# Kernel optimization log

Hardware: AMD Instinct MI355X
Metric: run time of the kernel (lower is better)

The kernel has to match this reference:

```python
import jax, jax.numpy as jnp
import numpy as np

NUM_HEADS = 16


def rotate_half(x):
    half = x.shape[-1] // 2
    return jnp.concatenate([-x[..., half:], x[..., :half]], axis=-1)


def setup_inputs() -> dict:
    key = jax.random.key(0)
    k0, k1, k2 = jax.random.split(key, 3)
    S, DIM, H = 16384, 1280, NUM_HEADS
    D = DIM // H            # 80
    G, L = 16, 1024         # 16 images, 1024 patch tokens each (S = G*L)

    hidden_states = jax.random.normal(k0, (S, DIM), dtype=jnp.float32) * 0.02

    # RoPE tables over packed positions
    pos = jnp.arange(S, dtype=jnp.float32)
    inv_freq = 1.0 / (10000.0 ** (jnp.arange(0, D, 2, dtype=jnp.float32) / D))
    freqs = pos[:, None] * inv_freq[None, :]          # [S, D/2]
    emb = jnp.concatenate([freqs, freqs], axis=-1)    # [S, D]
    cos = jnp.cos(emb)
    sin = jnp.sin(emb)

    cu_seqlens = (jnp.arange(G + 1, dtype=jnp.int32) * L)

    w_qkv = jax.random.normal(k1, (DIM, 3 * DIM), dtype=jnp.float32) * 0.02
    b_qkv = jnp.zeros((3 * DIM,), dtype=jnp.float32)
    w_proj = jax.random.normal(k2, (DIM, DIM), dtype=jnp.float32) * 0.02
    b_proj = jnp.zeros((DIM,), dtype=jnp.float32)

    return {
        "hidden_states": hidden_states,
        "cos": cos,
        "sin": sin,
        "w_qkv": w_qkv,
        "b_qkv": b_qkv,
        "w_proj": w_proj,
        "b_proj": b_proj,
        "cu_seqlens": cu_seqlens,
    }


def reference(hidden_states, cos, sin, w_qkv, b_qkv, w_proj, b_proj, cu_seqlens):
    S, DIM = hidden_states.shape
    H = NUM_HEADS
    D = DIM // H
    G = cu_seqlens.shape[0] - 1   # equal-length segments
    L = S // G

    qkv = (hidden_states @ w_qkv + b_qkv).reshape(S, 3, H, D)
    q, k, v = qkv[:, 0], qkv[:, 1], qkv[:, 2]   # [S, H, D]

    # RoPE (computed in fp32 as in source)
    c = cos[:, None, :]
    s = sin[:, None, :]
    q = q * c + rotate_half(q) * s
    k = k * c + rotate_half(k) * s

    # Source applies head_dim**-0.5 on q AND SDPA's default head_dim**-0.5,
    # so effective scale is head_dim**-1.
    scale = 1.0 / D

    qg = q.reshape(G, L, H, D)
    kg = k.reshape(G, L, H, D)
    vg = v.reshape(G, L, H, D)

    scores = jnp.einsum('glhd,gmhd->ghlm', qg, kg) * scale  # [G,H,L,L]
    attn = jax.nn.softmax(scores, axis=-1)
    out = jnp.einsum('ghlm,gmhd->glhd', attn, vg)           # [G,L,H,D]
    out = out.reshape(S, H * D)
    return out @ w_proj + b_proj
```

## Files before the change

### kernel.cpp

```cpp
#include <hip/hip_runtime.h>
#include <cmath>

#define SEQ   16384
#define DIMV  1280
#define NH    16
#define HD    80
#define NG    16
#define GL    1024
#define LDQKV (3*DIMV)

typedef short s16x8 __attribute__((ext_vector_type(8)));
typedef float f32x4 __attribute__((ext_vector_type(4)));

__device__ __forceinline__ unsigned short f2bf(float f) {
    union { float f; unsigned int u; } v; v.f = f;
    unsigned int u = v.u;
    return (unsigned short)((u + 0x7FFFu + ((u >> 16) & 1u)) >> 16);
}
__device__ __forceinline__ float bf2f(unsigned short h) {
    union { unsigned int u; float f; } v; v.u = ((unsigned int)h) << 16;
    return v.f;
}
__device__ __forceinline__ unsigned int pack2(float a, float b) {
    return (unsigned int)f2bf(a) | ((unsigned int)f2bf(b) << 16);
}
__device__ __forceinline__ void gload_lds16(const void* g, void* l) {
    __builtin_amdgcn_global_load_lds(
        (const __attribute__((address_space(1))) unsigned int*)g,
        (__attribute__((address_space(3))) unsigned int*)l,
        16, 0, 0);
}

__global__ __launch_bounds__(256) void convert_bf16_kernel(
    const float* __restrict__ src, unsigned short* __restrict__ dst, int n)
{
    int i = (blockIdx.x * 256 + threadIdx.x) * 8;
    if (i >= n) return;
    float4 a = *(const float4*)&src[i];
    float4 b = *(const float4*)&src[i + 4];
    uint4 o;
    o.x = pack2(a.x, a.y); o.y = pack2(a.z, a.w);
    o.z = pack2(b.x, b.y); o.w = pack2(b.z, b.w);
    *(uint4*)&dst[i] = o;
}

__global__ __launch_bounds__(256) void transpose_bf16_kernel(
    const float* __restrict__ W, unsigned short* __restrict__ WT,
    int Kdim, int N)
{
    __shared__ float tile[32][33];
    const int bx = blockIdx.x * 32;
    const int by = blockIdx.y * 32;
    const int tx = threadIdx.x & 31, ty = threadIdx.x >> 5;
#pragma unroll
    for (int j = 0; j < 4; ++j)
        tile[ty + j * 8][tx] = W[(size_t)(by + ty + j * 8) * N + bx + tx];
    __syncthreads();
#pragma unroll
    for (int j = 0; j < 4; ++j)
        WT[(size_t)(bx + ty + j * 8) * Kdim + by + tx] =
            f2bf(tile[tx][ty + j * 8]);
}

__global__ __launch_bounds__(256) void vtranspose_kernel(
    const unsigned short* __restrict__ qkv, unsigned short* __restrict__ vT)
{
    __shared__ unsigned short tile[128][88];
    const int t  = threadIdx.x;
    const int l0 = blockIdx.x * 128;
    const int gh = blockIdx.y;
    const int g  = gh >> 4, h = gh & 15;

#pragma unroll
    for (int s = 0; s < 5; ++s) {
        int i = t + s * 256;
        int row = i / 10, c = i % 10;
        *(uint4*)&tile[row][c * 8] = *(const uint4*)
            &qkv[(size_t)(g * GL + l0 + row) * LDQKV + 2 * DIMV + h * HD + c * 8];
    }
    __syncthreads();

#pragma unroll
    for (int s = 0; s < 5; ++s) {
        int i = t + s * 256;
        int d = i / 16, c16 = i % 16;
        uint4 o;
        o.x = (unsigned int)tile[c16 * 8 + 0][d] | ((unsigned int)tile[c16 * 8 + 1][d] << 16);
        o.y = (unsigned int)tile[c16 * 8 + 2][d] | ((unsigned int)tile[c16 * 8 + 3][d] << 16);
        o.z = (unsigned int)tile[c16 * 8 + 4][d] | ((unsigned int)tile[c16 * 8 + 5][d] << 16);
        o.w = (unsigned int)tile[c16 * 8 + 6][d] | ((unsigned int)tile[c16 * 8 + 7][d] << 16);
        *(uint4*)&vT[((size_t)gh * HD + d) * GL + l0 + c16 * 8] = o;
    }
}

template <bool BF16_OUT>
__global__ __launch_bounds__(512, 2) void gemm256_kernel(
    const unsigned short* __restrict__ A,
    const unsigned short* __restrict__ BT,
    const float* __restrict__ bias,
    void* __restrict__ C, int ldc, int K)
{
    __shared__ unsigned short As0[256 * 64], Bs0[256 * 64];
    __shared__ unsigned short As1[256 * 64], Bs1[256 * 64];

    const int t    = threadIdx.x;
    const int w    = t >> 6, lane = t & 63;
    const int wm   = w >> 2, wn = w & 3;
    const int gr   = lane >> 4, c15 = lane & 15;

    const int dd  = blockIdx.y * gridDim.x + blockIdx.x;
    const int cpx = (gridDim.x * gridDim.y) >> 3;
    const int sw  = (dd & 7) * cpx + (dd >> 3);
    const int bn  = (sw / gridDim.y) * 256;
    const int bm  = (sw % gridDim.y) * 256;

    const unsigned short* Ab = A  + (size_t)bm * K;
    const unsigned short* Bb = BT + (size_t)bn * K;
    const int NT = K >> 6;

    size_t soff[2]; int dstoff[2];
#pragma unroll
    for (int i = 0; i < 2; ++i) {
        int idx = t + i * 512, r = idx >> 3, blk = idx & 7;
        int cb  = blk ^ (r & 7);
        soff[i]   = ((size_t)r * K + cb * 8) * 2;
        dstoff[i] = idx * 16;
    }
    auto stage = [&](const unsigned short* src, unsigned short* ldsb,
                     int kt, int hh) {
#pragma unroll
        for (int i = 0; i < 2; ++i)
            gload_lds16((const char*)src + soff[i]
                            + (size_t)hh * ((size_t)128 * K * 2)
                            + (size_t)kt * 128,
                        (char*)ldsb + hh * 16384 + dstoff[i]);
    };

    f32x4 acc[8][4];
#pragma unroll
    for (int m = 0; m < 8; ++m)
#pragma unroll
        for (int n = 0; n < 4; ++n) acc[m][n] = (f32x4){0.f, 0.f, 0.f, 0.f};

    stage(Ab, As0, 0, 0); stage(Ab, As0, 0, 1);
    stage(Bb, Bs0, 0, 0); stage(Bb, Bs0, 0, 1);
    if (NT > 1) {
        stage(Bb, Bs1, 1, 0); stage(Bb, Bs1, 1, 1);
        asm volatile("s_waitcnt vmcnt(4)" ::: "memory");
    } else {
        asm volatile("s_waitcnt vmcnt(0)" ::: "memory");
    }
    __builtin_amdgcn_s_barrier();

    int cur = 0;
    for (int kt = 0; kt < NT; ++kt) {
        const unsigned short* Ac = cur ? As1 : As0;
        const unsigned short* Bc = cur ? Bs1 : Bs0;
        unsigned short* An  = cur ? As0 : As1;
        unsigned short* Bcw = cur ? Bs1 : Bs0;

        s16x8 bf[4][2];
#pragma unroll
        for (int p = 0; p < 4; ++p) {
            if (p == 0) {
#pragma unroll
                for (int n = 0; n < 4; ++n)
#pragma unroll
                    for (int k = 0; k < 2; ++k) {
                        int row = wn * 64 + n * 16 + c15;
                        bf[n][k] = *(const s16x8*)((const char*)Bc + row * 128
                                       + ((k * 64 + gr * 16) ^ ((row & 7) << 4)));
                    }
            }
            s16x8 af[2][2];
#pragma unroll
            for (int mi = 0; mi < 2; ++mi)
#pragma unroll
                for (int k = 0; k < 2; ++k) {
                    int row = wm * 128 + p * 32 + mi * 16 + c15;
                    af[mi][k] = *(const s16x8*)((const char*)Ac + row * 128
                                    + ((k * 64 + gr * 16) ^ ((row & 7) << 4)));
                }
            if (p == 0 && kt + 1 < NT) stage(Ab, An, kt + 1, 0);
            if (p == 1 && kt + 1 < NT) stage(Ab, An, kt + 1, 1);
            if (p == 2 && kt + 2 < NT) stage(Bb, Bcw, kt + 2, 0);
            if (p == 3 && kt + 2 < NT) stage(Bb, Bcw, kt + 2, 1);

            __builtin_amdgcn_s_barrier();
            asm volatile("s_waitcnt lgkmcnt(0)" ::: "memory");
            __builtin_amdgcn_sched_barrier(0);
            __builtin_amdgcn_s_setprio(1);
#pragma unroll
            for (int mi = 0; mi < 2; ++mi)
#pragma unroll
                for (int n = 0; n < 4; ++n)
#pragma unroll
                    for (int k = 0; k < 2; ++k)
                        acc[p * 2 + mi][n] = __builtin_amdgcn_mfma_f32_16x16x32_bf16(
                            af[mi][k], bf[n][k], acc[p * 2 + mi][n], 0, 0, 0);
            __builtin_amdgcn_s_setprio(0);
            if (p < 3) __builtin_amdgcn_s_barrier();
        }
        if (kt + 1 < NT) {
            if (kt + 2 < NT) asm volatile("s_waitcnt vmcnt(4)" ::: "memory");
            else             asm volatile("s_waitcnt vmcnt(0)" ::: "memory");
        }
        __builtin_amdgcn_s_barrier();
        cur ^= 1;
    }

#pragma unroll
    for (int m = 0; m < 8; ++m) {
        int row0 = bm + wm * 128 + m * 16 + gr * 4;
#pragma unroll
        for (int n = 0; n < 4; ++n) {
            int col = bn + wn * 64 + n * 16 + c15;
            float bv = bias[col];
#pragma unroll
            for (int j = 0; j < 4; ++j) {
                float v = acc[m][n][j] + bv;
                if (BF16_OUT)
                    ((unsigned short*)C)[(size_t)(row0 + j) * ldc + col] = f2bf(v);
                else
                    ((float*)C)[(size_t)(row0 + j) * ldc + col] = v;
            }
        }
    }
}

__global__ __launch_bounds__(256) void rope_bf16_kernel(
    unsigned short* __restrict__ qkv,
    const float* __restrict__ cos_t,
    const float* __restrict__ sin_t)
{
    int u = blockIdx.x * 256 + threadIdx.x;
    if (u >= SEQ * NH * 20) return;
    int s   = u / (NH * 20);
    int rem = u % (NH * 20);
    int h   = rem / 20;
    int d   = (rem % 20) * 2;

    float2 c  = *(const float2*)&cos_t[s * HD + d];
    float2 sn = *(const float2*)&sin_t[s * HD + d];
    size_t base = (size_t)s * LDQKV + h * HD + d;

#pragma unroll
    for (int part = 0; part < 2; ++part) {
        size_t b = base + part * DIMV;
        unsigned int lo = *(unsigned int*)&qkv[b];
        unsigned int hi = *(unsigned int*)&qkv[b + 40];
        float x0 = bf2f((unsigned short)lo), x1 = bf2f((unsigned short)(lo >> 16));
        float y0 = bf2f((unsigned short)hi), y1 = bf2f((unsigned short)(hi >> 16));
        *(unsigned int*)&qkv[b]      = pack2(x0 * c.x - y0 * sn.x, x1 * c.y - y1 * sn.y);
        *(unsigned int*)&qkv[b + 40] = pack2(y0 * c.x + x0 * sn.x, y1 * c.y + x1 * sn.y);
    }
}

__global__ __launch_bounds__(512) void attn_mfma_kernel(
    const unsigned short* __restrict__ qkv,
    const unsigned short* __restrict__ vT,
    unsigned short* __restrict__ ao)
{
    const int bx  = blockIdx.x;
    const int qt  = bx >> 8;
    const int ghi = bx & 255;
    const int h   = ghi & 15;
    const int g   = ghi >> 4;

    __shared__ unsigned short Ks[64][104];
    __shared__ unsigned short Vt[96][72];
    __shared__ unsigned short Pl[8][16][72];

    const int t    = threadIdx.x;
    const int w    = t >> 6;
    const int lane = t & 63;
    const int gr   = lane >> 4;
    const int c15  = lane & 15;

    const size_t qrow0 = (size_t)g * GL + (size_t)qt * 128;
    const unsigned short* kbase  = qkv + (size_t)g * GL * LDQKV + DIMV + h * HD;
    const unsigned short* vtbase = vT + (size_t)ghi * HD * GL;

    {
        int r = t >> 3, cp = t & 7;
        *(unsigned int*)&Ks[r][80 + cp * 2] = 0u;
    }
    for (int i = t; i < 16 * 36; i += 512) {
        int row = 80 + i / 36, c2 = i % 36;
        *(unsigned int*)&Vt[row][c2 * 2] = (row == 80) ? 0x3F803F80u : 0u;
    }

    const int  kA_r = t / 10,         kA_c = t % 10;
    const int  kB_r = (t + 512) / 10, kB_c = (t + 512) % 10;
    const int  vA_d = t >> 3,         vA_c = t & 7;
    const int  vB_d = 64 + (t >> 3);
    const bool two  = (t < 128);
    const size_t offKA = (size_t)kA_r * LDQKV + kA_c * 8;
    const size_t offKB = (size_t)kB_r * LDQKV + kB_c * 8;
    const size_t offVA = (size_t)vA_d * GL + vA_c * 8;
    const size_t offVB = (size_t)vB_d * GL + vA_c * 8;

    uint4 kra, krb, vra, vrb;
    kra = *(const uint4*)&kbase[offKA];
    vra = *(const uint4*)&vtbase[offVA];
    if (two) {
        krb = *(const uint4*)&kbase[offKB];
        vrb = *(const uint4*)&vtbase[offVB];
    }

    s16x8 qf[3];
    {
        const unsigned short* qp = qkv + (qrow0 + w * 16 + c15) * LDQKV + h * HD;
#pragma unroll
        for (int kk = 0; kk < 3; ++kk) {
            int d0 = kk * 32 + gr * 8;
            if (d0 < 80) qf[kk] = *(const s16x8*)&qp[d0];
            else         qf[kk] = (s16x8){0,0,0,0,0,0,0,0};
        }
    }

    f32x4 oacc[6];
#pragma unroll
    for (int nt = 0; nt < 6; ++nt) oacc[nt] = (f32x4){0.f, 0.f, 0.f, 0.f};

    const float SC = 1.0f / 80.0f;

    for (int kc = 0; kc < GL / 64; ++kc) {
        __syncthreads();

        *(uint4*)&Ks[kA_r][kA_c * 8] = kra;
        if (two) *(uint4*)&Ks[kB_r][kB_c * 8] = krb;
        *(uint4*)&Vt[vA_d][vA_c * 8] = vra;
        if (two) *(uint4*)&Vt[vB_d][vA_c * 8] = vrb;
        __syncthreads();

        if (kc + 1 < GL / 64) {
            const unsigned short* kb = kbase + (size_t)(kc + 1) * 64 * LDQKV;
            const unsigned short* vb = vtbase + (size_t)(kc + 1) * 64;
            kra = *(const uint4*)&kb[offKA];
            vra = *(const uint4*)&vb[offVA];
            if (two) {
                krb = *(const uint4*)&kb[offKB];
                vrb = *(const uint4*)&vb[offVB];
            }
        }

        f32x4 s[4];
#pragma unroll
        for (int nt = 0; nt < 4; ++nt) {
            f32x4 a = (f32x4){0.f, 0.f, 0.f, 0.f};
#pragma unroll
            for (int kk = 0; kk < 3; ++kk) {
                s16x8 kfrag = *(const s16x8*)&Ks[nt * 16 + c15][kk * 32 + gr * 8];
                a = __builtin_amdgcn_mfma_f32_16x16x32_bf16(qf[kk], kfrag, a, 0, 0, 0);
            }
            s[nt] = a;
        }

#pragma unroll
        for (int nt = 0; nt < 4; ++nt)
#pragma unroll
            for (int r = 0; r < 4; ++r)
                Pl[w][gr * 4 + r][nt * 16 + c15] = f2bf(__expf(s[nt][r] * SC));
        asm volatile("s_waitcnt lgkmcnt(0)" ::: "memory");
        __builtin_amdgcn_sched_barrier(0);
        s16x8 pa0 = *(const s16x8*)&Pl[w][c15][gr * 8];
        s16x8 pa1 = *(const s16x8*)&Pl[w][c15][32 + gr * 8];

#pragma unroll
        for (int nt = 0; nt < 6; ++nt) {
            s16x8 vf0 = *(const s16x8*)&Vt[nt * 16 + c15][gr * 8];
            s16x8 vf1 = *(const s16x8*)&Vt[nt * 16 + c15][32 + gr * 8];
            f32x4 o = oacc[nt];
            o = __builtin_amdgcn_mfma_f32_16x16x32_bf16(pa0, vf0, o, 0, 0, 0);
            o = __builtin_amdgcn_mfma_f32_16x16x32_bf16(pa1, vf1, o, 0, 0, 0);
            oacc[nt] = o;
        }
    }

    float inv[4];
#pragma unroll
    for (int r = 0; r < 4; ++r)
        inv[r] = 1.0f / __shfl(oacc[5][r], lane & 48);
    const size_t orow0 = qrow0 + w * 16;
#pragma unroll
    for (int nt = 0; nt < 5; ++nt)
#pragma unroll
        for (int r = 0; r < 4; ++r)
            ao[(orow0 + gr * 4 + r) * DIMV + h * HD + nt * 16 + c15] =
                f2bf(oacc[nt][r] * inv[r]);
}

extern "C" void kernel_launch(void* const* d_in, const int* in_sizes, int n_in,
                              void* d_out, int out_size, void* d_ws, size_t ws_size,
                              hipStream_t stream)
{
    const float* hidden = (const float*)d_in[0];
    const float* cos_t  = (const float*)d_in[1];
    const float* sin_t  = (const float*)d_in[2];
    const float* w_qkv  = (const float*)d_in[3];
    const float* b_qkv  = (const float*)d_in[4];
    const float* w_proj = (const float*)d_in[5];
    const float* b_proj = (const float*)d_in[6];

    float* out = (float*)d_out;

    char* ws = (char*)d_ws;
    unsigned short* qkv_bf = (unsigned short*)(ws);
    unsigned short* hbf    = (unsigned short*)(ws + 125829120);
    unsigned short* vT     = (unsigned short*)(ws + 125829120);
    unsigned short* ao_bf  = (unsigned short*)(ws + 167772160);
    unsigned short* wqkvT  = (unsigned short*)(ws + 209715200);
    unsigned short* wprojT = (unsigned short*)(ws + 219545600);

    {
        int n = SEQ * DIMV;
        convert_bf16_kernel<<<n / 8 / 256, 256, 0, stream>>>(hidden, hbf, n);
        transpose_bf16_kernel<<<dim3(3 * DIMV / 32, DIMV / 32), 256, 0, stream>>>(
            w_qkv, wqkvT, DIMV, 3 * DIMV);
        transpose_bf16_kernel<<<dim3(DIMV / 32, DIMV / 32), 256, 0, stream>>>(
            w_proj, wprojT, DIMV, DIMV);
    }
    gemm256_kernel<true><<<dim3(3 * DIMV / 256, SEQ / 256), 512, 0, stream>>>(
        hbf, wqkvT, b_qkv, qkv_bf, 3 * DIMV, DIMV);
    {
        int n = SEQ * NH * 20;
        rope_bf16_kernel<<<n / 256, 256, 0, stream>>>(qkv_bf, cos_t, sin_t);
    }
    vtranspose_kernel<<<dim3(GL / 128, NG * NH), 256, 0, stream>>>(qkv_bf, vT);
    attn_mfma_kernel<<<dim3(NG * NH * (GL / 128)), 512, 0, stream>>>(
        qkv_bf, vT, ao_bf);
    gemm256_kernel<false><<<dim3(DIMV / 256, SEQ / 256), 512, 0, stream>>>(
        ao_bf, wprojT, b_proj, out, DIMV, DIMV);
}
```

Measured before the change: 651.2 us.

## Double query rows per attention block to reuse K/V tiles across two Q tiles

Each wave now processes two 16-row query tiles instead of one, so each attention block covers 256 query rows and the grid is halved. Every K and V fragment loaded from shared memory feeds two MFMAs, which halves the global and LDS traffic for K/V per query row. The cost is more registers for the doubled accumulators and Q fragments (launch bounds now request 4 blocks) and half as many blocks, which may reduce occupancy and load balance.

```diff
diff --git a/kernel.cpp b/kernel.cpp
--- a/kernel.cpp
+++ b/kernel.cpp
@@ -256,7 +256,7 @@
     }
 }
 
-__global__ __launch_bounds__(512) void attn_mfma_kernel(
+__global__ __launch_bounds__(512, 4) void attn_mfma_kernel(
     const unsigned short* __restrict__ qkv,
     const unsigned short* __restrict__ vT,
     unsigned short* __restrict__ ao)
@@ -269,7 +269,7 @@
 
     __shared__ unsigned short Ks[64][104];
     __shared__ unsigned short Vt[96][72];
-    __shared__ unsigned short Pl[8][16][72];
+    __shared__ unsigned short Pl[8][32][72];
 
     const int t    = threadIdx.x;
     const int w    = t >> 6;
@@ -277,7 +277,7 @@
     const int gr   = lane >> 4;
     const int c15  = lane & 15;
 
-    const size_t qrow0 = (size_t)g * GL + (size_t)qt * 128;
+    const size_t qrow0 = (size_t)g * GL + (size_t)qt * 256;
     const unsigned short* kbase  = qkv + (size_t)g * GL * LDQKV + DIMV + h * HD;
     const unsigned short* vtbase = vT + (size_t)ghi * HD * GL;
 
@@ -308,20 +308,24 @@
         vrb = *(const uint4*)&vtbase[offVB];
     }
 
-    s16x8 qf[3];
-    {
-        const unsigned short* qp = qkv + (qrow0 + w * 16 + c15) * LDQKV + h * HD;
+    s16x8 qf[2][3];
+#pragma unroll
+    for (int qq = 0; qq < 2; ++qq) {
+        const unsigned short* qp =
+            qkv + (qrow0 + w * 32 + qq * 16 + c15) * LDQKV + h * HD;
 #pragma unroll
         for (int kk = 0; kk < 3; ++kk) {
             int d0 = kk * 32 + gr * 8;
-            if (d0 < 80) qf[kk] = *(const s16x8*)&qp[d0];
-            else         qf[kk] = (s16x8){0,0,0,0,0,0,0,0};
-        }
-    }
-
-    f32x4 oacc[6];
-#pragma unroll
-    for (int nt = 0; nt < 6; ++nt) oacc[nt] = (f32x4){0.f, 0.f, 0.f, 0.f};
+            if (d0 < 80) qf[qq][kk] = *(const s16x8*)&qp[d0];
+            else         qf[qq][kk] = (s16x8){0,0,0,0,0,0,0,0};
+        }
+    }
+
+    f32x4 oacc[2][6];
+#pragma unroll
+    for (int qq = 0; qq < 2; ++qq)
+#pragma unroll
+        for (int nt = 0; nt < 6; ++nt) oacc[qq][nt] = (f32x4){0.f,0.f,0.f,0.f};
 
     const float SC = 1.0f / 80.0f;
 
@@ -345,50 +349,70 @@
             }
         }
 
-        f32x4 s[4];
+        f32x4 s[2][4];
 #pragma unroll
         for (int nt = 0; nt < 4; ++nt) {
-            f32x4 a = (f32x4){0.f, 0.f, 0.f, 0.f};
-#pragma unroll
-            for (int kk = 0; kk < 3; ++kk) {
-                s16x8 kfrag = *(const s16x8*)&Ks[nt * 16 + c15][kk * 32 + gr * 8];
-                a = __builtin_amdgcn_mfma_f32_16x16x32_bf16(qf[kk], kfrag, a, 0, 0, 0);
+            s16x8 kfr[3];
+#pragma unroll
+            for (int kk = 0; kk < 3; ++kk)
+                kfr[kk] = *(const s16x8*)&Ks[nt * 16 + c15][kk * 32 + gr * 8];
+#pragma unroll
+            for (int qq = 0; qq < 2; ++qq) {
+                f32x4 a = (f32x4){0.f, 0.f, 0.f, 0.f};
+#pragma unroll
+                for (int kk = 0; kk < 3; ++kk)
+                    a = __builtin_amdgcn_mfma_f32_16x16x32_bf16(
+                        qf[qq][kk], kfr[kk], a, 0, 0, 0);
+                s[qq][nt] = a;
             }
-            s[nt] = a;
-        }
-
-#pragma unroll
-        for (int nt = 0; nt < 4; ++nt)
-#pragma unroll
-            for (int r = 0; r < 4; ++r)
-                Pl[w][gr * 4 + r][nt * 16 + c15] = f2bf(__expf(s[nt][r] * SC));
+        }
+
+#pragma unroll
+        for (int qq = 0; qq < 2; ++qq)
+#pragma unroll
+            for (int nt = 0; nt < 4; ++nt)
+#pragma unroll
+                for (int r = 0; r < 4; ++r)
+                    Pl[w][qq * 16 + gr * 4 + r][nt * 16 + c15] =
+                        f2bf(__expf(s[qq][nt][r] * SC));
         asm volatile("s_waitcnt lgkmcnt(0)" ::: "memory");
         __builtin_amdgcn_sched_barrier(0);
-        s16x8 pa0 = *(const s16x8*)&Pl[w][c15][gr * 8];
-        s16x8 pa1 = *(const s16x8*)&Pl[w][c15][32 + gr * 8];
+
+        s16x8 pa[2][2];
+#pragma unroll
+        for (int qq = 0; qq < 2; ++qq) {
+            pa[qq][0] = *(const s16x8*)&Pl[w][qq * 16 + c15][gr * 8];
+            pa[qq][1] = *(const s16x8*)&Pl[w][qq * 16 + c15][32 + gr * 8];
+        }
 
 #pragma unroll
         for (int nt = 0; nt < 6; ++nt) {
             s16x8 vf0 = *(const s16x8*)&Vt[nt * 16 + c15][gr * 8];
             s16x8 vf1 = *(const s16x8*)&Vt[nt * 16 + c15][32 + gr * 8];
-            f32x4 o = oacc[nt];
-            o = __builtin_amdgcn_mfma_f32_16x16x32_bf16(pa0, vf0, o, 0, 0, 0);
-            o = __builtin_amdgcn_mfma_f32_16x16x32_bf16(pa1, vf1, o, 0, 0, 0);
-            oacc[nt] = o;
-        }
-    }
-
-    float inv[4];
-#pragma unroll
-    for (int r = 0; r < 4; ++r)
-        inv[r] = 1.0f / __shfl(oacc[5][r], lane & 48);
-    const size_t orow0 = qrow0 + w * 16;
-#pragma unroll
-    for (int nt = 0; nt < 5; ++nt)
+#pragma unroll
+            for (int qq = 0; qq < 2; ++qq) {
+                f32x4 o = oacc[qq][nt];
+                o = __builtin_amdgcn_mfma_f32_16x16x32_bf16(pa[qq][0], vf0, o, 0, 0, 0);
+                o = __builtin_amdgcn_mfma_f32_16x16x32_bf16(pa[qq][1], vf1, o, 0, 0, 0);
+                oacc[qq][nt] = o;
+            }
+        }
+    }
+
+#pragma unroll
+    for (int qq = 0; qq < 2; ++qq) {
+        float inv[4];
 #pragma unroll
         for (int r = 0; r < 4; ++r)
-            ao[(orow0 + gr * 4 + r) * DIMV + h * HD + nt * 16 + c15] =
-                f2bf(oacc[nt][r] * inv[r]);
+            inv[r] = 1.0f / __shfl(oacc[qq][5][r], lane & 48);
+        const size_t orow0 = qrow0 + w * 32 + qq * 16;
+#pragma unroll
+        for (int nt = 0; nt < 5; ++nt)
+#pragma unroll
+            for (int r = 0; r < 4; ++r)
+                ao[(orow0 + gr * 4 + r) * DIMV + h * HD + nt * 16 + c15] =
+                    f2bf(oacc[qq][nt][r] * inv[r]);
+    }
 }
 
 extern "C" void kernel_launch(void* const* d_in, const int* in_sizes, int n_in,
@@ -428,7 +452,7 @@
         rope_bf16_kernel<<<n / 256, 256, 0, stream>>>(qkv_bf, cos_t, sin_t);
     }
     vtranspose_kernel<<<dim3(GL / 128, NG * NH), 256, 0, stream>>>(qkv_bf, vT);
-    attn_mfma_kernel<<<dim3(NG * NH * (GL / 128)), 512, 0, stream>>>(
+    attn_mfma_kernel<<<dim3(NG * NH * (GL / 256)), 512, 0, stream>>>(
         qkv_bf, vT, ao_bf);
     gemm256_kernel<false><<<dim3(DIMV / 256, SEQ / 256), 512, 0, stream>>>(
         ao_bf, wprojT, b_proj, out, DIMV, DIMV);
```

After: 633.8 us. -2.7%, faster.
